# Kernel tuning notes

Hardware: AMD Instinct MI355X
Metric: run time of the kernel (lower is better)

The kernel has to match this reference:

```python
import jax, jax.numpy as jnp
import numpy as np

N = 8192
MAX_ITER = 128
THRESHOLD = 0.0
EPS = 1e-6


def setup_inputs() -> dict:
    key = jax.random.key(0)
    k1, k2, k3 = jax.random.split(key, 3)
    x = jax.random.normal(k1, (N,), dtype=jnp.float32)
    weight = jax.random.normal(k2, (N, N), dtype=jnp.float32)
    bias = jax.random.normal(k3, (N,), dtype=jnp.float32)
    return {"x": x, "weight": weight, "bias": bias}


def reference(x, weight, bias):
    # Faithful port of HopfieldNet._run: synchronous sign update with
    # energy-based early stopping, unrolled as a masked lax.scan so the
    # result matches the Python loop that returns as soon as |dE| < eps.
    def energy(v):
        # e = -0.5 * v @ W @ v - b @ v
        return -0.5 * (v @ (weight @ v)) - bias @ v

    e0 = energy(x)

    def step(carry, _):
        xc, ec, done = carry
        # F.linear(x, W, b) for 1-D x == W @ x + b
        x_new = jnp.sign(weight @ xc + bias - THRESHOLD)
        e_new = energy(x_new)
        conv = jnp.abs(e_new - ec) < EPS
        x_out = jnp.where(done, xc, x_new)
        e_out = jnp.where(done, ec, e_new)
        return (x_out, e_out, done | conv), None

    (x_final, _, _), _ = jax.lax.scan(
        step, (x, e0, jnp.array(False)), None, length=MAX_ITER
    )
    return x_final
```

## Files before the change

kernel.cpp:

```cpp
#include <hip/hip_runtime.h>

#define N 8192
#define MAX_ITER 128
#define EPS 1e-6f
#define TAU_I8 12.0f
#define TAU_R  0.05f
#define QINV   0.0625f
#define RINV   (1.0f/4096.0f)
#define NPART  2048

#if defined(__has_builtin)
#  if __has_builtin(__builtin_amdgcn_sdot4)
#    define SDOT4(a,b,c) __builtin_amdgcn_sdot4((a),(b),(c),false)
#  endif
#endif
#ifndef SDOT4
static __device__ __forceinline__ int sdot4_sw(int a, int b, int c) {
    c += (int)(signed char)(a & 0xff)       * (int)(signed char)(b & 0xff);
    c += (int)(signed char)((a>>8) & 0xff)  * (int)(signed char)((b>>8) & 0xff);
    c += (int)(signed char)((a>>16) & 0xff) * (int)(signed char)((b>>16) & 0xff);
    c += (int)(signed char)((a>>24) & 0xff) * (int)(signed char)((b>>24) & 0xff);
    return c;
}
#define SDOT4(a,b,c) sdot4_sw((a),(b),(c))
#endif

__device__ __forceinline__ float sgnf(float v) {
    return (v > 0.f) ? 1.f : ((v < 0.f) ? -1.f : 0.f);
}

__global__ __launch_bounds__(256) void init_kernel(float* __restrict__ eacc,
                                                   int* __restrict__ done,
                                                   int* __restrict__ satflag) {
    int i = blockIdx.x * 256 + threadIdx.x;
    if (i < N) satflag[i] = 0;
    if (i < MAX_ITER) eacc[i] = 0.f;
    if (i == 0) *done = 0;
}

__global__ __launch_bounds__(256) void compress_kernel(const float* __restrict__ W,
                                                       signed char* __restrict__ Wq,
                                                       signed char* __restrict__ Rq,
                                                       int* __restrict__ satflag) {
    const size_t base = ((size_t)blockIdx.x * 256 + threadIdx.x) * 16;
    const float4* w4 = (const float4*)(W + base);
    int sat = 0;
    uint4 oq, orr;
    unsigned* pq = (unsigned*)&oq;
    unsigned* pr = (unsigned*)&orr;
    #pragma unroll
    for (int v = 0; v < 4; ++v) {
        float4 w = w4[v];
        unsigned uq = 0, ur = 0;
        const float* e = (const float*)&w;
        #pragma unroll
        for (int k = 0; k < 4; ++k) {
            int q = __float2int_rn(e[k] * 16.0f);
            if (q > 127)  { q = 127;  sat = 1; }
            if (q < -127) { q = -127; sat = 1; }
            float r = e[k] - (float)q * QINV;
            int rq = __float2int_rn(r * 4096.0f);
            if (rq > 127)  rq = 127;
            if (rq < -127) rq = -127;
            uq |= ((unsigned)(q & 0xff)) << (8 * k);
            ur |= ((unsigned)(rq & 0xff)) << (8 * k);
        }
        pq[v] = uq; pr[v] = ur;
    }
    *(uint4*)(Wq + base) = oq;
    *(uint4*)(Rq + base) = orr;
    if (sat) atomicOr(&satflag[base >> 13], 1);
}

__global__ __launch_bounds__(512, 4)
void t0_kernel(const float* __restrict__ W,
               const float* __restrict__ bias,
               const float* __restrict__ x0,
               signed char* __restrict__ xout,
               float* __restrict__ pout) {
    __shared__ float xs[N];
    __shared__ float esum[8];
    const int tid = threadIdx.x;
    {
        const float4* x4 = (const float4*)x0;
        float4* s4 = (float4*)xs;
        for (int i = tid; i < N / 4; i += 512) s4[i] = x4[i];
    }
    __syncthreads();
    const int wave = tid >> 6;
    const int lane = tid & 63;
    const int row  = ((int)blockIdx.x << 3) + wave;
    const float4* Wr  = (const float4*)(W + (size_t)row * N);
    const float4* xs4 = (const float4*)xs;
    float a0 = 0.f, a1 = 0.f, a2 = 0.f, a3 = 0.f;
    #pragma unroll
    for (int p = 0; p < 8; ++p) {
        int j = p * 256 + lane;
        float4 w0 = Wr[j];         float4 q0 = xs4[j];
        float4 w1 = Wr[j + 64];    float4 q1 = xs4[j + 64];
        float4 w2 = Wr[j + 128];   float4 q2 = xs4[j + 128];
        float4 w3 = Wr[j + 192];   float4 q3 = xs4[j + 192];
        a0 += w0.x * q0.x + w0.y * q0.y + w0.z * q0.z + w0.w * q0.w;
        a1 += w1.x * q1.x + w1.y * q1.y + w1.z * q1.z + w1.w * q1.w;
        a2 += w2.x * q2.x + w2.y * q2.y + w2.z * q2.z + w2.w * q2.w;
        a3 += w3.x * q3.x + w3.y * q3.y + w3.z * q3.z + w3.w * q3.w;
    }
    float tot = (a0 + a1) + (a2 + a3);
    #pragma unroll
    for (int off = 32; off > 0; off >>= 1) tot += __shfl_down(tot, off);
    if (lane == 0) {
        const float br = bias[row];
        const float v = tot + br;
        xout[row] = (signed char)((v > 0.f) ? 1 : ((v < 0.f) ? -1 : 0));
        const float xr = xs[row];
        esum[wave] = -0.5f * xr * tot - br * xr;
    }
    __syncthreads();
    if (tid == 0) {
        float s = ((esum[0] + esum[1]) + (esum[2] + esum[3])) +
                  ((esum[4] + esum[5]) + (esum[6] + esum[7]));
        pout[blockIdx.x] = s;
        pout[1024 + blockIdx.x] = 0.f;
    }
}

__global__ __launch_bounds__(256, 8)
void step_kernel(const signed char* __restrict__ Wq,
                 const signed char* __restrict__ Rq,
                 const float* __restrict__ W,
                 const float* __restrict__ bias,
                 const unsigned* __restrict__ xin,
                 signed char* __restrict__ xout,
                 const float* __restrict__ pin,
                 float* __restrict__ pout,
                 float* __restrict__ eacc,
                 const int* __restrict__ satflag,
                 int t,
                 int* __restrict__ done) {
    if (*done) return;

    __shared__ unsigned xq[2048];
    __shared__ float red[256];
    __shared__ float esum[4];

    const int tid  = threadIdx.x;
    const int wave = tid >> 6;
    const int lane = tid & 63;
    const int row  = ((int)blockIdx.x << 2) + wave;

    const uint4* Wr = (const uint4*)(Wq + (size_t)row * N);
    uint4 wq[8];
    #pragma unroll
    for (int p = 0; p < 8; ++p) wq[p] = Wr[(p << 6) + lane];

    {
        const uint4* xg4 = (const uint4*)xin;
        uint4* xs4w = (uint4*)xq;
        xs4w[tid]       = xg4[tid];
        xs4w[tid + 256] = xg4[tid + 256];
    }
    float s = 0.f;
    #pragma unroll
    for (int k = 0; k < 8; ++k) s += pin[(tid << 3) + k];
    red[tid] = s;
    __syncthreads();
    #pragma unroll
    for (int off = 128; off > 0; off >>= 1) {
        if (tid < off) red[tid] += red[tid + off];
        __syncthreads();
    }
    const float E = red[0];

    if (t >= 2 && fabsf(E - eacc[t - 2]) < EPS) {
        if (blockIdx.x == 0 && tid == 0) *done = 1 + ((t - 1) & 1);
        return;
    }
    if (blockIdx.x == 0 && tid == 0) eacc[t - 1] = E;

    const uint4* xs4 = (const uint4*)xq;
    int acc = 0;
    #pragma unroll
    for (int p = 0; p < 8; ++p) {
        const uint4 xv = xs4[(p << 6) + lane];
        const uint4 w  = wq[p];
        acc = SDOT4((int)w.x, (int)xv.x, acc);
        acc = SDOT4((int)w.y, (int)xv.y, acc);
        acc = SDOT4((int)w.z, (int)xv.z, acc);
        acc = SDOT4((int)w.w, (int)xv.w, acc);
    }
    #pragma unroll
    for (int off = 1; off < 64; off <<= 1) acc += __shfl_xor(acc, off);

    const float br  = bias[row];
    const int   sat = satflag[row];
    float yfin = (float)acc * QINV;

    if (fabsf(yfin + br) < TAU_I8 || sat) {
        const uint4* Rr = (const uint4*)(Rq + (size_t)row * N);
        int racc = 0;
        #pragma unroll
        for (int p = 0; p < 8; ++p) {
            const uint4 xv = xs4[(p << 6) + lane];
            const uint4 w  = Rr[(p << 6) + lane];
            racc = SDOT4((int)w.x, (int)xv.x, racc);
            racc = SDOT4((int)w.y, (int)xv.y, racc);
            racc = SDOT4((int)w.z, (int)xv.z, racc);
            racc = SDOT4((int)w.w, (int)xv.w, racc);
        }
        #pragma unroll
        for (int off = 1; off < 64; off <<= 1) racc += __shfl_xor(racc, off);
        yfin = (float)acc * QINV + (float)racc * RINV;

        if (fabsf(yfin + br) < TAU_R || sat) {
            const float4* Wf = (const float4*)(W + (size_t)row * N);
            float b0 = 0.f, b1 = 0.f, b2 = 0.f, b3 = 0.f;
            #pragma unroll
            for (int p = 0; p < 8; ++p) {
                const int j = p * 256 + lane;
                #pragma unroll
                for (int c = 0; c < 4; ++c) {
                    const int idx = j + c * 64;
                    const float4 w = Wf[idx];
                    const unsigned u = xq[idx];
                    float4 q;
                    q.x = (float)(signed char)(u & 0xff);
                    q.y = (float)(signed char)((u >> 8) & 0xff);
                    q.z = (float)(signed char)((u >> 16) & 0xff);
                    q.w = (float)(signed char)(u >> 24);
                    const float d = w.x * q.x + w.y * q.y + w.z * q.z + w.w * q.w;
                    if (c == 0) b0 += d; else if (c == 1) b1 += d;
                    else if (c == 2) b2 += d; else b3 += d;
                }
            }
            float tot = (b0 + b1) + (b2 + b3);
            #pragma unroll
            for (int off = 32; off > 0; off >>= 1) tot += __shfl_down(tot, off);
            yfin = tot;
        }
    }

    if (lane == 0) {
        const float v = yfin + br;
        xout[row] = (signed char)((v > 0.f) ? 1 : ((v < 0.f) ? -1 : 0));
        const float xr = (float)(signed char)((xq[row >> 2] >> ((row & 3) * 8)) & 0xff);
        esum[wave] = -0.5f * xr * yfin - br * xr;
    }
    __syncthreads();
    if (tid == 0)
        pout[blockIdx.x] = (esum[0] + esum[1]) + (esum[2] + esum[3]);
}

__global__ __launch_bounds__(256)
void out_kernel(const signed char* __restrict__ xpk0,
                const signed char* __restrict__ xpk1,
                const float* __restrict__ pin1,
                const float* __restrict__ eacc,
                const int* __restrict__ done,
                float* __restrict__ out) {
    __shared__ float red[256];
    const int tid = threadIdx.x;
    const int d = *done;
    float4* o4 = (float4*)out;

    const signed char* xf;
    if (d) {
        xf = (d - 1) ? xpk1 : xpk0;
    } else {
        float s = 0.f;
        #pragma unroll
        for (int k = 0; k < 8; ++k) s += pin1[(tid << 3) + k];
        red[tid] = s;
        __syncthreads();
        #pragma unroll
        for (int off = 128; off > 0; off >>= 1) {
            if (tid < off) red[tid] += red[tid + off];
            __syncthreads();
        }
        const bool conv = fabsf(red[0] - eacc[126]) < EPS;
        xf = conv ? xpk1 : xpk0;
    }
    const char4* p4 = (const char4*)xf;
    for (int i = tid; i < N / 4; i += 256) {
        char4 c = p4[i];
        o4[i] = make_float4((float)c.x, (float)c.y, (float)c.z, (float)c.w);
    }
}

__global__ __launch_bounds__(256) void fb_init(float* __restrict__ eacc,
                                               int* __restrict__ done) {
    int i = threadIdx.x;
    if (i <= MAX_ITER) eacc[i] = 0.0f;
    if (i == 0) *done = 0;
}

__global__ __launch_bounds__(512, 4) void fb_mv(const float* __restrict__ W,
                                                const float* __restrict__ bias,
                                                const float* __restrict__ x0,
                                                const signed char* __restrict__ xin,
                                                signed char* __restrict__ xnext,
                                                float* __restrict__ eacc,
                                                int t,
                                                int* __restrict__ done) {
    if (t >= 2) {
        if (*done) return;
        float d = fabsf(eacc[t - 1] - eacc[t - 2]);
        if (d < EPS) {
            if (threadIdx.x == 0) *done = 1 + ((t - 1) & 1);
            return;
        }
    }
    __shared__ float xs[N];
    __shared__ float wsum[8];
    if (t == 0) {
        const float4* x4 = (const float4*)x0;
        float4* s4 = (float4*)xs;
        for (int i = threadIdx.x; i < N / 4; i += 512) s4[i] = x4[i];
    } else {
        #pragma unroll
        for (int k = 0; k < 16; ++k) {
            int e = threadIdx.x + k * 512;
            xs[e] = (float)xin[e];
        }
    }
    __syncthreads();
    const int wave = threadIdx.x >> 6;
    const int lane = threadIdx.x & 63;
    const int row  = ((int)blockIdx.x << 3) + wave;
    const float4* Wr  = (const float4*)(W + (size_t)row * N);
    const float4* xs4 = (const float4*)xs;
    float a0 = 0.f, a1 = 0.f, a2 = 0.f, a3 = 0.f;
    #pragma unroll
    for (int p = 0; p < 8; ++p) {
        int j = p * 256 + lane;
        float4 w0 = Wr[j];         float4 q0 = xs4[j];
        float4 w1 = Wr[j + 64];    float4 q1 = xs4[j + 64];
        float4 w2 = Wr[j + 128];   float4 q2 = xs4[j + 128];
        float4 w3 = Wr[j + 192];   float4 q3 = xs4[j + 192];
        a0 += w0.x * q0.x + w0.y * q0.y + w0.z * q0.z + w0.w * q0.w;
        a1 += w1.x * q1.x + w1.y * q1.y + w1.z * q1.z + w1.w * q1.w;
        a2 += w2.x * q2.x + w2.y * q2.y + w2.z * q2.z + w2.w * q2.w;
        a3 += w3.x * q3.x + w3.y * q3.y + w3.z * q3.z + w3.w * q3.w;
    }
    float tot = (a0 + a1) + (a2 + a3);
    #pragma unroll
    for (int off = 32; off > 0; off >>= 1) tot += __shfl_down(tot, off);
    if (lane == 0) {
        float br = bias[row];
        float v = tot + br;
        xnext[row] = (signed char)((v > 0.f) ? 1 : ((v < 0.f) ? -1 : 0));
        float xr = xs[row];
        wsum[wave] = -0.5f * xr * tot - br * xr;
    }
    __syncthreads();
    if (threadIdx.x == 0) {
        float s = 0.f;
        #pragma unroll
        for (int w = 0; w < 8; ++w) s += wsum[w];
        atomicAdd(&eacc[t], s);
    }
}

__global__ __launch_bounds__(256) void fb_out(const signed char* __restrict__ p0,
                                              const signed char* __restrict__ p1,
                                              const int* __restrict__ done,
                                              float* __restrict__ out) {
    int i = blockIdx.x * 256 + threadIdx.x;
    int d = *done;
    const signed char* p = d ? ((d - 1) ? p1 : p0) : p0;
    out[i] = (float)p[i];
}

extern "C" void kernel_launch(void* const* d_in, const int* in_sizes, int n_in,
                              void* d_out, int out_size, void* d_ws, size_t ws_size,
                              hipStream_t stream) {
    const float* x0 = (const float*)d_in[0];
    const float* W  = (const float*)d_in[1];
    const float* b  = (const float*)d_in[2];
    float* out = (float*)d_out;

    char* p = (char*)d_ws;
    signed char* Wq = (signed char*)p;        p += (size_t)N * N;
    signed char* Rq = (signed char*)p;        p += (size_t)N * N;
    signed char* xpk0 = (signed char*)p;      p += N;
    signed char* xpk1 = (signed char*)p;      p += N;
    float* partial = (float*)p;               p += 2 * NPART * sizeof(float);
    float* eacc = (float*)p;                  p += MAX_ITER * sizeof(float);
    int*   satflag = (int*)p;                 p += N * sizeof(int);
    int*   done = (int*)p;                    p += 16;
    const size_t needed = (size_t)(p - (char*)d_ws);

    if (ws_size >= needed) {
        init_kernel<<<N / 256, 256, 0, stream>>>(eacc, done, satflag);
        compress_kernel<<<(int)((size_t)N * N / (256 * 16)), 256, 0, stream>>>(W, Wq, Rq, satflag);
        t0_kernel<<<N / 8, 512, 0, stream>>>(W, b, x0, xpk1, partial);
        for (int t = 1; t < MAX_ITER; ++t) {
            const unsigned* xin  = (const unsigned*)((t & 1) ? xpk1 : xpk0);
            signed char*    xout = ((t + 1) & 1) ? xpk1 : xpk0;
            const float*    pin  = partial + ((t - 1) & 1) * NPART;
            float*          pout = partial + (t & 1) * NPART;
            step_kernel<<<NPART, 256, 0, stream>>>(Wq, Rq, W, b, xin, xout,
                                                   pin, pout, eacc, satflag, t, done);
        }
        out_kernel<<<1, 256, 0, stream>>>(xpk0, xpk1, partial + NPART, eacc, done, out);
    } else {
        float*       feacc = (float*)d_ws;
        int*         fdone = (int*)(feacc + MAX_ITER + 2);
        signed char* p0    = (signed char*)(fdone + 16);
        signed char* p1    = p0 + N;
        fb_init<<<1, 256, 0, stream>>>(feacc, fdone);
        for (int t = 0; t <= MAX_ITER; ++t) {
            const signed char* xin   = (t & 1) ? p1 : p0;
            signed char*       xnext = (t & 1) ? p0 : p1;
            fb_mv<<<N / 8, 512, 0, stream>>>(W, b, x0, xin, xnext, feacc, t, fdone);
        }
        fb_out<<<N / 256, 256, 0, stream>>>(p0, p1, fdone, out);
    }
}
```

Before: 3.341 ms.

## Use incremental sparse matvec over flipped neurons with transposed int8 weights

Replaces the full int8 matvec each iteration with an incremental update: the weights are stored transposed, and each step accumulates only the columns of neurons whose sign changed, added to a persistent integer pre-activation. Convergence is detected as a zero flip count instead of an energy comparison, which removes the per-step energy reduction. This cuts weight traffic per iteration when few neurons flip, at the cost of an extra kernel launch per step, a 64-way partial-sum buffer, and atomics to build the change list. The zero-flip test stands in for the energy-difference test and can stop at a different step than the reference in edge cases.

```diff
diff --git a/kernel.cpp b/kernel.cpp
--- a/kernel.cpp
+++ b/kernel.cpp
@@ -7,7 +7,8 @@
 #define TAU_R  0.05f
 #define QINV   0.0625f
 #define RINV   (1.0f/4096.0f)
-#define NPART  2048
+#define GRP    64
+#define SEGS   32
 
 #if defined(__has_builtin)
 #  if __has_builtin(__builtin_amdgcn_sdot4)
@@ -25,32 +26,34 @@
 #define SDOT4(a,b,c) sdot4_sw((a),(b),(c))
 #endif
 
-__device__ __forceinline__ float sgnf(float v) {
-    return (v > 0.f) ? 1.f : ((v < 0.f) ? -1.f : 0.f);
-}
-
-__global__ __launch_bounds__(256) void init_kernel(float* __restrict__ eacc,
-                                                   int* __restrict__ done,
-                                                   int* __restrict__ satflag) {
-    int i = blockIdx.x * 256 + threadIdx.x;
-    if (i < N) satflag[i] = 0;
-    if (i < MAX_ITER) eacc[i] = 0.f;
-    if (i == 0) *done = 0;
-}
-
-__global__ __launch_bounds__(256) void compress_kernel(const float* __restrict__ W,
-                                                       signed char* __restrict__ Wq,
-                                                       signed char* __restrict__ Rq,
-                                                       int* __restrict__ satflag) {
-    const size_t base = ((size_t)blockIdx.x * 256 + threadIdx.x) * 16;
-    const float4* w4 = (const float4*)(W + base);
+__global__ __launch_bounds__(256) void init_kernel(int* __restrict__ yint,
+                                                   int* __restrict__ satflag,
+                                                   int* __restrict__ cnt,
+                                                   int* __restrict__ done) {
+    const int i = blockIdx.x * 256 + threadIdx.x;
+    yint[i] = 0;
+    satflag[i] = 0;
+    if (i == 0) { cnt[0] = 0; cnt[1] = 0; *done = 0; }
+}
+
+__global__ __launch_bounds__(256)
+void compressT_kernel(const float* __restrict__ W,
+                      signed char* __restrict__ WqT,
+                      signed char* __restrict__ Rq,
+                      int* __restrict__ satflag) {
+    __shared__ unsigned tq[64][17];
+    const int bid = blockIdx.x;
+    const int ti = bid >> 7, tj = bid & 127;
+    const int i0 = ti << 6, j0 = tj << 6;
+    const int tid = threadIdx.x;
+    const int r  = tid >> 2, q4 = tid & 3;
+    const float4* wrow = (const float4*)(W + (size_t)(i0 + r) * N + j0 + (q4 << 4));
     int sat = 0;
-    uint4 oq, orr;
-    unsigned* pq = (unsigned*)&oq;
+    uint4 orr;
     unsigned* pr = (unsigned*)&orr;
     #pragma unroll
     for (int v = 0; v < 4; ++v) {
-        float4 w = w4[v];
+        float4 w = wrow[v];
         unsigned uq = 0, ur = 0;
         const float* e = (const float*)&w;
         #pragma unroll
@@ -58,28 +61,39 @@
             int q = __float2int_rn(e[k] * 16.0f);
             if (q > 127)  { q = 127;  sat = 1; }
             if (q < -127) { q = -127; sat = 1; }
-            float r = e[k] - (float)q * QINV;
-            int rq = __float2int_rn(r * 4096.0f);
+            float rr = e[k] - (float)q * QINV;
+            int rq = __float2int_rn(rr * 4096.0f);
             if (rq > 127)  rq = 127;
             if (rq < -127) rq = -127;
             uq |= ((unsigned)(q & 0xff)) << (8 * k);
             ur |= ((unsigned)(rq & 0xff)) << (8 * k);
         }
-        pq[v] = uq; pr[v] = ur;
-    }
-    *(uint4*)(Wq + base) = oq;
-    *(uint4*)(Rq + base) = orr;
-    if (sat) atomicOr(&satflag[base >> 13], 1);
+        pr[v] = ur;
+        tq[r][(q4 << 2) + v] = uq;
+    }
+    *(uint4*)(Rq + (size_t)(i0 + r) * N + j0 + (q4 << 4)) = orr;
+    if (sat) atomicOr(&satflag[i0 + r], 1);
+    __syncthreads();
+    const int c = tid >> 2, qq = tid & 3;
+    unsigned ob[4];
+    #pragma unroll
+    for (int v = 0; v < 4; ++v) {
+        const int rb = (qq << 4) + (v << 2);
+        const unsigned b0 = (tq[rb + 0][c >> 2] >> ((c & 3) * 8)) & 0xff;
+        const unsigned b1 = (tq[rb + 1][c >> 2] >> ((c & 3) * 8)) & 0xff;
+        const unsigned b2 = (tq[rb + 2][c >> 2] >> ((c & 3) * 8)) & 0xff;
+        const unsigned b3 = (tq[rb + 3][c >> 2] >> ((c & 3) * 8)) & 0xff;
+        ob[v] = b0 | (b1 << 8) | (b2 << 16) | (b3 << 24);
+    }
+    *(uint4*)(WqT + (size_t)(j0 + c) * N + i0 + (qq << 4)) = *(uint4*)ob;
 }
 
 __global__ __launch_bounds__(512, 4)
 void t0_kernel(const float* __restrict__ W,
                const float* __restrict__ bias,
                const float* __restrict__ x0,
-               signed char* __restrict__ xout,
-               float* __restrict__ pout) {
+               signed char* __restrict__ xout) {
     __shared__ float xs[N];
-    __shared__ float esum[8];
     const int tid = threadIdx.x;
     {
         const float4* x4 = (const float4*)x0;
@@ -109,92 +123,104 @@
     #pragma unroll
     for (int off = 32; off > 0; off >>= 1) tot += __shfl_down(tot, off);
     if (lane == 0) {
-        const float br = bias[row];
-        const float v = tot + br;
+        const float v = tot + bias[row];
         xout[row] = (signed char)((v > 0.f) ? 1 : ((v < 0.f) ? -1 : 0));
-        const float xr = xs[row];
-        esum[wave] = -0.5f * xr * tot - br * xr;
-    }
-    __syncthreads();
-    if (tid == 0) {
-        float s = ((esum[0] + esum[1]) + (esum[2] + esum[3])) +
-                  ((esum[4] + esum[5]) + (esum[6] + esum[7]));
-        pout[blockIdx.x] = s;
-        pout[1024 + blockIdx.x] = 0.f;
     }
 }
 
 __global__ __launch_bounds__(256, 8)
-void step_kernel(const signed char* __restrict__ Wq,
-                 const signed char* __restrict__ Rq,
-                 const float* __restrict__ W,
-                 const float* __restrict__ bias,
-                 const unsigned* __restrict__ xin,
-                 signed char* __restrict__ xout,
-                 const float* __restrict__ pin,
-                 float* __restrict__ pout,
-                 float* __restrict__ eacc,
-                 const int* __restrict__ satflag,
-                 int t,
-                 int* __restrict__ done) {
+void accum_kernel(const signed char* __restrict__ WqT,
+                  const signed char* __restrict__ xcur,
+                  const int* __restrict__ list,
+                  const int* __restrict__ count,
+                  int* __restrict__ nextcount,
+                  int* __restrict__ ypart,
+                  const int* __restrict__ done,
+                  int dense) {
     if (*done) return;
-
-    __shared__ unsigned xq[2048];
-    __shared__ float red[256];
-    __shared__ float esum[4];
-
+    const int tid = threadIdx.x;
+    if (blockIdx.x == 0 && tid == 0) *nextcount = 0;
+    const int g = blockIdx.x >> 5;
+    const int s = blockIdx.x & 31;
+    const int seg0 = s << 8;
+    const int wave = tid >> 6, lane = tid & 63;
+    __shared__ int elist[128];
+    __shared__ int red[4][256];
+    int nc;
+    if (dense) {
+        nc = 128;
+    } else {
+        const int k = *count;
+        const int cpg = (k + 63) >> 6;
+        const int beg = g * cpg;
+        nc = k - beg; if (nc < 0) nc = 0; if (nc > cpg) nc = cpg;
+        for (int e = tid; e < nc; e += 256) elist[e] = list[beg + e];
+    }
+    __syncthreads();
+    int a0 = 0, a1 = 0, a2 = 0, a3 = 0;
+    if (dense) {
+        for (int e = wave; e < nc; e += 4) {
+            const int j = (g << 7) + e;
+            const int d = (int)xcur[j];
+            const unsigned w = *(const unsigned*)(WqT + (size_t)j * N + seg0 + (lane << 2));
+            a0 += d * (int)(signed char)(w & 0xff);
+            a1 += d * (int)(signed char)((w >> 8) & 0xff);
+            a2 += d * (int)(signed char)((w >> 16) & 0xff);
+            a3 += d * (int)(signed char)(w >> 24);
+        }
+    } else {
+        for (int e = wave; e < nc; e += 4) {
+            const int en = elist[e];
+            const int j = en >> 3;
+            const int d = (en & 7) - 2;
+            const unsigned w = *(const unsigned*)(WqT + (size_t)j * N + seg0 + (lane << 2));
+            a0 += d * (int)(signed char)(w & 0xff);
+            a1 += d * (int)(signed char)((w >> 8) & 0xff);
+            a2 += d * (int)(signed char)((w >> 16) & 0xff);
+            a3 += d * (int)(signed char)(w >> 24);
+        }
+    }
+    *(int4*)&red[wave][lane << 2] = make_int4(a0, a1, a2, a3);
+    __syncthreads();
+    const int v = (red[0][tid] + red[1][tid]) + (red[2][tid] + red[3][tid]);
+    ypart[(g << 13) + seg0 + tid] = v;
+}
+
+__global__ __launch_bounds__(256, 8)
+void decide_kernel(const signed char* __restrict__ Rq,
+                   const float* __restrict__ W,
+                   const float* __restrict__ bias,
+                   const signed char* __restrict__ xin,
+                   signed char* __restrict__ xout,
+                   const int* __restrict__ ypart,
+                   int* __restrict__ yint,
+                   const int* __restrict__ count,
+                   int* __restrict__ nlist,
+                   int* __restrict__ ncount,
+                   const int* __restrict__ satflag,
+                   int t,
+                   int* __restrict__ done) {
+    if (*done) return;
+    if (t >= 2 && *count == 0) {
+        if (blockIdx.x == 0 && threadIdx.x == 0) *done = 1 + (t & 1);
+        return;
+    }
     const int tid  = threadIdx.x;
     const int wave = tid >> 6;
     const int lane = tid & 63;
     const int row  = ((int)blockIdx.x << 2) + wave;
 
-    const uint4* Wr = (const uint4*)(Wq + (size_t)row * N);
-    uint4 wq[8];
-    #pragma unroll
-    for (int p = 0; p < 8; ++p) wq[p] = Wr[(p << 6) + lane];
-
-    {
-        const uint4* xg4 = (const uint4*)xin;
-        uint4* xs4w = (uint4*)xq;
-        xs4w[tid]       = xg4[tid];
-        xs4w[tid + 256] = xg4[tid + 256];
-    }
-    float s = 0.f;
-    #pragma unroll
-    for (int k = 0; k < 8; ++k) s += pin[(tid << 3) + k];
-    red[tid] = s;
-    __syncthreads();
-    #pragma unroll
-    for (int off = 128; off > 0; off >>= 1) {
-        if (tid < off) red[tid] += red[tid + off];
-        __syncthreads();
-    }
-    const float E = red[0];
-
-    if (t >= 2 && fabsf(E - eacc[t - 2]) < EPS) {
-        if (blockIdx.x == 0 && tid == 0) *done = 1 + ((t - 1) & 1);
-        return;
-    }
-    if (blockIdx.x == 0 && tid == 0) eacc[t - 1] = E;
-
-    const uint4* xs4 = (const uint4*)xq;
-    int acc = 0;
-    #pragma unroll
-    for (int p = 0; p < 8; ++p) {
-        const uint4 xv = xs4[(p << 6) + lane];
-        const uint4 w  = wq[p];
-        acc = SDOT4((int)w.x, (int)xv.x, acc);
-        acc = SDOT4((int)w.y, (int)xv.y, acc);
-        acc = SDOT4((int)w.z, (int)xv.z, acc);
-        acc = SDOT4((int)w.w, (int)xv.w, acc);
-    }
-    #pragma unroll
-    for (int off = 1; off < 64; off <<= 1) acc += __shfl_xor(acc, off);
+    int yp = ypart[(lane << 13) + row];
+    #pragma unroll
+    for (int off = 32; off > 0; off >>= 1) yp += __shfl_xor(yp, off);
+    const int acc = yint[row] + yp;
+    if (lane == 0) yint[row] = acc;
 
     const float br  = bias[row];
     const int   sat = satflag[row];
     float yfin = (float)acc * QINV;
 
+    const uint4* xs4 = (const uint4*)xin;
     if (fabsf(yfin + br) < TAU_I8 || sat) {
         const uint4* Rr = (const uint4*)(Rq + (size_t)row * N);
         int racc = 0;
@@ -213,6 +239,7 @@
 
         if (fabsf(yfin + br) < TAU_R || sat) {
             const float4* Wf = (const float4*)(W + (size_t)row * N);
+            const unsigned* xw = (const unsigned*)xin;
             float b0 = 0.f, b1 = 0.f, b2 = 0.f, b3 = 0.f;
             #pragma unroll
             for (int p = 0; p < 8; ++p) {
@@ -221,7 +248,7 @@
                 for (int c = 0; c < 4; ++c) {
                     const int idx = j + c * 64;
                     const float4 w = Wf[idx];
-                    const unsigned u = xq[idx];
+                    const unsigned u = xw[idx];
                     float4 q;
                     q.x = (float)(signed char)(u & 0xff);
                     q.y = (float)(signed char)((u >> 8) & 0xff);
@@ -241,49 +268,27 @@
 
     if (lane == 0) {
         const float v = yfin + br;
-        xout[row] = (signed char)((v > 0.f) ? 1 : ((v < 0.f) ? -1 : 0));
-        const float xr = (float)(signed char)((xq[row >> 2] >> ((row & 3) * 8)) & 0xff);
-        esum[wave] = -0.5f * xr * yfin - br * xr;
-    }
-    __syncthreads();
-    if (tid == 0)
-        pout[blockIdx.x] = (esum[0] + esum[1]) + (esum[2] + esum[3]);
+        const signed char nv = (signed char)((v > 0.f) ? 1 : ((v < 0.f) ? -1 : 0));
+        xout[row] = nv;
+        const signed char ov = xin[row];
+        if (nv != ov) {
+            const int d = (int)nv - (int)ov;
+            const int idx = atomicAdd(ncount, 1);
+            nlist[idx] = (row << 3) | ((d + 2) & 7);
+        }
+    }
 }
 
 __global__ __launch_bounds__(256)
 void out_kernel(const signed char* __restrict__ xpk0,
                 const signed char* __restrict__ xpk1,
-                const float* __restrict__ pin1,
-                const float* __restrict__ eacc,
                 const int* __restrict__ done,
                 float* __restrict__ out) {
-    __shared__ float red[256];
-    const int tid = threadIdx.x;
     const int d = *done;
-    float4* o4 = (float4*)out;
-
-    const signed char* xf;
-    if (d) {
-        xf = (d - 1) ? xpk1 : xpk0;
-    } else {
-        float s = 0.f;
-        #pragma unroll
-        for (int k = 0; k < 8; ++k) s += pin1[(tid << 3) + k];
-        red[tid] = s;
-        __syncthreads();
-        #pragma unroll
-        for (int off = 128; off > 0; off >>= 1) {
-            if (tid < off) red[tid] += red[tid + off];
-            __syncthreads();
-        }
-        const bool conv = fabsf(red[0] - eacc[126]) < EPS;
-        xf = conv ? xpk1 : xpk0;
-    }
-    const char4* p4 = (const char4*)xf;
-    for (int i = tid; i < N / 4; i += 256) {
-        char4 c = p4[i];
-        o4[i] = make_float4((float)c.x, (float)c.y, (float)c.z, (float)c.w);
-    }
+    const signed char* xf = d ? ((d - 1) ? xpk1 : xpk0) : xpk0;
+    const int i = blockIdx.x * 256 + threadIdx.x;
+    const char4 c = ((const char4*)xf)[i];
+    ((float4*)out)[i] = make_float4((float)c.x, (float)c.y, (float)c.z, (float)c.w);
 }
 
 __global__ __launch_bounds__(256) void fb_init(float* __restrict__ eacc,
@@ -379,29 +384,42 @@
     float* out = (float*)d_out;
 
     char* p = (char*)d_ws;
-    signed char* Wq = (signed char*)p;        p += (size_t)N * N;
-    signed char* Rq = (signed char*)p;        p += (size_t)N * N;
+    signed char* WqT = (signed char*)p;       p += (size_t)N * N;
+    signed char* Rq  = (signed char*)p;       p += (size_t)N * N;
     signed char* xpk0 = (signed char*)p;      p += N;
     signed char* xpk1 = (signed char*)p;      p += N;
-    float* partial = (float*)p;               p += 2 * NPART * sizeof(float);
-    float* eacc = (float*)p;                  p += MAX_ITER * sizeof(float);
-    int*   satflag = (int*)p;                 p += N * sizeof(int);
-    int*   done = (int*)p;                    p += 16;
+    int* yint = (int*)p;                      p += N * sizeof(int);
+    int* ypart = (int*)p;                     p += (size_t)GRP * N * sizeof(int);
+    int* list0 = (int*)p;                     p += N * sizeof(int);
+    int* list1 = (int*)p;                     p += N * sizeof(int);
+    int* satflag = (int*)p;                   p += N * sizeof(int);
+    int* cnt = (int*)p;                       p += 16;
+    int* done = (int*)p;                      p += 16;
     const size_t needed = (size_t)(p - (char*)d_ws);
 
     if (ws_size >= needed) {
-        init_kernel<<<N / 256, 256, 0, stream>>>(eacc, done, satflag);
-        compress_kernel<<<(int)((size_t)N * N / (256 * 16)), 256, 0, stream>>>(W, Wq, Rq, satflag);
-        t0_kernel<<<N / 8, 512, 0, stream>>>(W, b, x0, xpk1, partial);
-        for (int t = 1; t < MAX_ITER; ++t) {
-            const unsigned* xin  = (const unsigned*)((t & 1) ? xpk1 : xpk0);
-            signed char*    xout = ((t + 1) & 1) ? xpk1 : xpk0;
-            const float*    pin  = partial + ((t - 1) & 1) * NPART;
-            float*          pout = partial + (t & 1) * NPART;
-            step_kernel<<<NPART, 256, 0, stream>>>(Wq, Rq, W, b, xin, xout,
-                                                   pin, pout, eacc, satflag, t, done);
-        }
-        out_kernel<<<1, 256, 0, stream>>>(xpk0, xpk1, partial + NPART, eacc, done, out);
+        init_kernel<<<N / 256, 256, 0, stream>>>(yint, satflag, cnt, done);
+        compressT_kernel<<<(N / 64) * (N / 64), 256, 0, stream>>>(W, WqT, Rq, satflag);
+        t0_kernel<<<N / 8, 512, 0, stream>>>(W, b, x0, xpk1);
+        accum_kernel<<<GRP * SEGS, 256, 0, stream>>>(WqT, xpk1, list0, cnt + 1,
+                                                     cnt + 0, ypart, done, 1);
+        decide_kernel<<<N / 4, 256, 0, stream>>>(Rq, W, b, xpk1, xpk0, ypart, yint,
+                                                 cnt + 1, list0, cnt + 0, satflag,
+                                                 1, done);
+        for (int t = 2; t < MAX_ITER; ++t) {
+            const int cur = t & 1;
+            const signed char* xin = cur ? xpk1 : xpk0;
+            signed char* xo        = cur ? xpk0 : xpk1;
+            int* lcur = cur ? list1 : list0;
+            int* lnxt = cur ? list0 : list1;
+            accum_kernel<<<GRP * SEGS, 256, 0, stream>>>(WqT, xin, lcur, cnt + cur,
+                                                         cnt + (cur ^ 1), ypart,
+                                                         done, 0);
+            decide_kernel<<<N / 4, 256, 0, stream>>>(Rq, W, b, xin, xo, ypart, yint,
+                                                     cnt + cur, lnxt, cnt + (cur ^ 1),
+                                                     satflag, t, done);
+        }
+        out_kernel<<<N / 4 / 256, 256, 0, stream>>>(xpk0, xpk1, done, out);
     } else {
         float*       feacc = (float*)d_ws;
         int*         fdone = (int*)(feacc + MAX_ITER + 2);
```

Result: slower. 8.473 ms (+153.6%).
